# Performance work log

Measured on AMD Instinct MI355X. Metric: run time of the kernel, lower is better.

The kernel has to match this reference:

```python
import jax, jax.numpy as jnp
import numpy as np


def _pairwise_sqdist(a, b):
    # a: [m, n, d], b: [m, n, d] -> M: [m, n, n], M[m,i,j] = ||a[m,i]-b[m,j]||^2
    # Use the expansion |a|^2 + |b|^2 - 2 a.b to avoid materializing the
    # [m, n, n, d] difference tensor; clamp tiny negatives from cancellation.
    a2 = jnp.sum(a * a, axis=-1)  # [m, n]
    b2 = jnp.sum(b * b, axis=-1)  # [m, n]
    ab = jnp.einsum('mid,mjd->mij', a, b)  # [m, n, n]
    return jnp.maximum(a2[:, :, None] + b2[:, None, :] - 2.0 * ab, 0.0)


def setup_inputs() -> dict:
    key = jax.random.key(0)
    k1, k2 = jax.random.split(key)
    template = jax.random.normal(k1, (16, 4096, 3), dtype=jnp.float32)
    source = jax.random.normal(k2, (16, 4096, 3), dtype=jnp.float32)
    return {"template": template, "source": source}


def reference(template, source):
    M = _pairwise_sqdist(template, source)  # [m, n, n]
    # min over template index (axis 1): nearest template point for each source point
    dist1 = jnp.mean(jnp.sqrt(jnp.min(M, axis=1)))
    # min over source index (axis 2): nearest source point for each template point
    dist2 = jnp.mean(jnp.sqrt(jnp.min(M, axis=2)))
    return (dist1 + dist2) / 2.0
```

## Files before the change

### kernel.cpp

```cpp
#include <hip/hip_runtime.h>

#define N_PTS   4096
#define N_BATCH 16
#define INV_CNT (1.0f / (2.0f * N_BATCH * N_PTS))
#define AROW_BYTES ((size_t)2 * N_BATCH * N_PTS * 16 * 2)
#define NBLK    512

typedef _Float16 f16x8  __attribute__((ext_vector_type(8)));
#define AS1 __attribute__((address_space(1)))
#define AS3 __attribute__((address_space(3)))

__global__ __launch_bounds__(256) void prep_kernel(
    const float* __restrict__ tpl, const float* __restrict__ src,
    _Float16* __restrict__ arow, float* __restrict__ out) {
    int pt = blockIdx.x * 256 + threadIdx.x;
    if (pt == 0) out[0] = 0.0f;
    const float* p = (pt < 65536 ? tpl : src) + (size_t)(pt & 65535) * 3;
    float x = p[0], y = p[1], z = p[2];
    float o2 = fmaf(x, x, fmaf(y, y, z * z));
    _Float16 xh = (_Float16)x, yh = (_Float16)y, zh = (_Float16)z;
    _Float16 xl = (_Float16)(x - (float)xh);
    _Float16 yl = (_Float16)(y - (float)yh);
    _Float16 zl = (_Float16)(z - (float)zh);
    _Float16 o2h = (_Float16)o2;
    _Float16 o2l = (_Float16)(o2 - (float)o2h);
    const _Float16 m2 = (_Float16)-2.0f;
    f16x8 v0, v1;
    v0[0] = m2 * xh; v0[1] = m2 * yh; v0[2] = m2 * zh;
    v0[3] = m2 * xl; v0[4] = m2 * yl; v0[5] = m2 * zl;
    v0[6] = m2 * xh; v0[7] = m2 * yh;
    v1[0] = m2 * zh; v1[1] = o2h; v1[2] = o2l;
    v1[3] = (_Float16)0.0f; v1[4] = (_Float16)0.0f; v1[5] = (_Float16)0.0f;
    v1[6] = (_Float16)0.0f; v1[7] = (_Float16)0.0f;
    *(f16x8*)(arow + (size_t)pt * 16)     = v0;
    *(f16x8*)(arow + (size_t)pt * 16 + 8) = v1;
}

#define FD(a,x,y) "v_min3_f32 %[" #a "], v" #x ", v" #y ", %[" #a "]\n\t"
#define FOLD_A FD(acc0,32,33) FD(acc1,34,35) FD(acc0,36,37) FD(acc1,38,39) \
               FD(acc0,40,41) FD(acc1,42,43) FD(acc0,44,45) FD(acc1,46,47) \
               FD(acc2,64,65) FD(acc3,66,67) FD(acc2,68,69) FD(acc3,70,71) \
               FD(acc2,72,73) FD(acc3,74,75) FD(acc2,76,77) FD(acc3,78,79)
#define FOLD_B FD(acc0,48,49) FD(acc1,50,51) FD(acc0,52,53) FD(acc1,54,55) \
               FD(acc0,56,57) FD(acc1,58,59) FD(acc0,60,61) FD(acc1,62,63) \
               FD(acc2,80,81) FD(acc3,82,83) FD(acc2,84,85) FD(acc3,86,87) \
               FD(acc2,88,89) FD(acc3,90,91) FD(acc2,92,93) FD(acc3,94,95)
#define MF_A(d) \
  "v_mfma_f32_32x32x16_f16 v[32:47], %[" #d "], %[bf0], v[96:111]\n\t" \
  "v_mfma_f32_32x32x16_f16 v[64:79], %[" #d "], %[bf1], v[96:111]\n\t"
#define MF_B(d) \
  "v_mfma_f32_32x32x16_f16 v[48:63], %[" #d "], %[bf0], v[96:111]\n\t" \
  "v_mfma_f32_32x32x16_f16 v[80:95], %[" #d "], %[bf1], v[96:111]\n\t"
#define DSR(d,off) "ds_read_b128 %[" #d "], %[dsa] offset:" #off "\n\t"
#define WL(n) "s_waitcnt lgkmcnt(" #n ")\n\t"
#define ZM(r) "v_mov_b32 v" #r ", 0\n\t"
#define NOP3 "s_nop 7\n\t" "s_nop 7\n\t" "s_nop 7\n\t"

__global__ __launch_bounds__(256, 2) void chamfer_mfma(
    const float* __restrict__ tpl, const float* __restrict__ src,
    const _Float16* __restrict__ arow, float* __restrict__ blocksum,
    float* __restrict__ out) {
    __shared__ uint4 sbuf[2][1024];
    __shared__ float wsum[4];

    const int tid = threadIdx.x;
    const int wv = tid >> 6, lane = tid & 63;
    const int n = lane & 31, g = lane >> 5;
    const int lin = blockIdx.x + 16 * (blockIdx.y + 16 * blockIdx.z);
    const int s_  = lin >> 3;
    const int qb  = s_ & 15;
    const int region = (lin & 7) + 8 * (s_ >> 4);
    const int batch  = region & 15;
    const int dir    = region >> 4;

    const float* qpts = (dir == 0) ? src : tpl;
    const _Float16* abase = arow + ((dir == 0) ? (size_t)0 : (size_t)65536 * 16)
                          + (size_t)batch * 4096 * 16;

    f16x8 bfr[2];
    float p2[2];
    #pragma unroll
    for (int i = 0; i < 2; ++i) {
        const int q = qb * 256 + wv * 64 + i * 32 + n;
        const float* p = qpts + (size_t)(batch * 4096 + q) * 3;
        float px = p[0], py = p[1], pz = p[2];
        p2[i] = fmaf(px, px, fmaf(py, py, pz * pz));
        _Float16 xh = (_Float16)px, yh = (_Float16)py, zh = (_Float16)pz;
        _Float16 xl = (_Float16)(px - (float)xh);
        _Float16 yl = (_Float16)(py - (float)yh);
        _Float16 zl = (_Float16)(pz - (float)zh);
        f16x8 b;
        if (g == 0) {
            b[0] = xh; b[1] = yh; b[2] = zh;
            b[3] = xh; b[4] = yh; b[5] = zh;
            b[6] = xl; b[7] = yl;
        } else {
            b[0] = zl; b[1] = (_Float16)1.0f; b[2] = (_Float16)1.0f;
            b[3] = (_Float16)0.0f; b[4] = (_Float16)0.0f; b[5] = (_Float16)0.0f;
            b[6] = (_Float16)0.0f; b[7] = (_Float16)0.0f;
        }
        bfr[i] = b;
    }

    const int lane_off = n * 32 + g * 16;
    const unsigned dsa0 = (unsigned)(size_t)((AS3 char*)&sbuf[0][0]) + lane_off;
    const unsigned dsa1 = (unsigned)(size_t)((AS3 char*)&sbuf[1][0]) + lane_off;

    const char* gwave = (const char*)abase + wv * 4096 + lane * 16;
    #define STAGE(ch)                                                          \
        {                                                                      \
            const char* gp = gwave + (size_t)(ch) * 16384;                     \
            AS3 char* lp = (AS3 char*)&sbuf[(ch) & 1][0] + wv * 4096;          \
            _Pragma("unroll")                                                  \
            for (int j = 0; j < 4; ++j)                                        \
                __builtin_amdgcn_global_load_lds(                              \
                    (const AS1 unsigned*)(gp + j * 1024),                      \
                    (AS3 unsigned*)(lp + j * 1024), 16, 0, 0);                 \
        }

    float acc0 = 1e30f, acc1 = 1e30f, acc2 = 1e30f, acc3 = 1e30f;
    f16x8 d0, d1, d2, d3;

    STAGE(0)
    #pragma unroll 1
    for (int c = 0; c < 8; ++c) {
        if (c < 7) STAGE(c + 1)
        if (c < 7)
            asm volatile("s_waitcnt vmcnt(4)\n\ts_barrier" ::: "memory");
        else
            asm volatile("s_waitcnt vmcnt(0)\n\ts_barrier" ::: "memory");
        const unsigned dsa = (c & 1) ? dsa1 : dsa0;

        asm volatile(
            ZM(96) ZM(97) ZM(98) ZM(99) ZM(100) ZM(101) ZM(102) ZM(103)
            ZM(104) ZM(105) ZM(106) ZM(107) ZM(108) ZM(109) ZM(110) ZM(111)
            DSR(d0,0) DSR(d1,1024) DSR(d2,2048) DSR(d3,3072)
            WL(3) MF_A(d0) DSR(d0,4096) NOP3
            WL(3) MF_B(d1) DSR(d1,5120)  FOLD_A
            WL(3) MF_A(d2) DSR(d2,6144)  FOLD_B
            WL(3) MF_B(d3) DSR(d3,7168)  FOLD_A
            WL(3) MF_A(d0) DSR(d0,8192)  FOLD_B
            WL(3) MF_B(d1) DSR(d1,9216)  FOLD_A
            WL(3) MF_A(d2) DSR(d2,10240) FOLD_B
            WL(3) MF_B(d3) DSR(d3,11264) FOLD_A
            WL(3) MF_A(d0) DSR(d0,12288) FOLD_B
            WL(3) MF_B(d1) DSR(d1,13312) FOLD_A
            WL(3) MF_A(d2) DSR(d2,14336) FOLD_B
            WL(3) MF_B(d3) DSR(d3,15360) FOLD_A
            WL(3) MF_A(d0) FOLD_B
            WL(2) MF_B(d1) FOLD_A
            WL(1) MF_A(d2) FOLD_B
            WL(0) MF_B(d3) FOLD_A
            NOP3 FOLD_B
            : [d0]"=&v"(d0), [d1]"=&v"(d1), [d2]"=&v"(d2), [d3]"=&v"(d3),
              [acc0]"+v"(acc0), [acc1]"+v"(acc1),
              [acc2]"+v"(acc2), [acc3]"+v"(acc3)
            : [bf0]"v"(bfr[0]), [bf1]"v"(bfr[1]), [dsa]"v"(dsa)
            : "memory",
              "v32","v33","v34","v35","v36","v37","v38","v39",
              "v40","v41","v42","v43","v44","v45","v46","v47",
              "v48","v49","v50","v51","v52","v53","v54","v55",
              "v56","v57","v58","v59","v60","v61","v62","v63",
              "v64","v65","v66","v67","v68","v69","v70","v71",
              "v72","v73","v74","v75","v76","v77","v78","v79",
              "v80","v81","v82","v83","v84","v85","v86","v87",
              "v88","v89","v90","v91","v92","v93","v94","v95",
              "v96","v97","v98","v99","v100","v101","v102","v103",
              "v104","v105","v106","v107","v108","v109","v110","v111");

        asm volatile("s_barrier" ::: "memory");
    }

    float v0 = fminf(acc0, acc1);
    v0 = fminf(v0, __shfl_xor(v0, 32));
    float v1 = fminf(acc2, acc3);
    v1 = fminf(v1, __shfl_xor(v1, 32));
    float dd0 = fmaxf(v0 + p2[0], 0.0f);
    float dd1 = fmaxf(v1 + p2[1], 0.0f);
    float s = (sqrtf(dd0) + sqrtf(dd1)) * INV_CNT;
    if (g != 0) s = 0.0f;
    #pragma unroll
    for (int off = 32; off > 0; off >>= 1) s += __shfl_down(s, off);
    if (lane == 0) wsum[wv] = s;
    __syncthreads();
    if (tid == 0) {
        float t = wsum[0] + wsum[1] + wsum[2] + wsum[3];
        if (blocksum) {
            int flat = (dir * N_BATCH + batch) * 16 + qb;
            blocksum[flat] = t;
        } else {
            atomicAdd(out, t);
        }
    }
}

__global__ __launch_bounds__(256) void final_kernel(
    const float* __restrict__ blocksum, float* __restrict__ out) {
    __shared__ float wsum[4];
    float s = 0.0f;
    #pragma unroll
    for (int j = 0; j < NBLK / 256; ++j)
        s += blocksum[j * 256 + threadIdx.x];
    #pragma unroll
    for (int off = 32; off > 0; off >>= 1) s += __shfl_down(s, off);
    if ((threadIdx.x & 63) == 0) wsum[threadIdx.x >> 6] = s;
    __syncthreads();
    if (threadIdx.x == 0) out[0] = wsum[0] + wsum[1] + wsum[2] + wsum[3];
}

extern "C" void kernel_launch(void* const* d_in, const int* in_sizes, int n_in,
                              void* d_out, int out_size, void* d_ws, size_t ws_size,
                              hipStream_t stream) {
    const float* tpl = (const float*)d_in[0];
    const float* src = (const float*)d_in[1];
    float* out = (float*)d_out;
    _Float16* arow = (_Float16*)d_ws;
    const bool roomy = ws_size >= AROW_BYTES + NBLK * sizeof(float);
    float* blocksum = roomy ? (float*)((char*)d_ws + AROW_BYTES) : nullptr;

    hipLaunchKernelGGL(prep_kernel, dim3((2 * N_BATCH * N_PTS) / 256),
                       dim3(256), 0, stream, tpl, src, arow, out);
    dim3 grid(N_PTS / 256, N_BATCH, 2);
    hipLaunchKernelGGL(chamfer_mfma, grid, dim3(256), 0, stream,
                       tpl, src, arow, blocksum, out);
    if (roomy)
        hipLaunchKernelGGL(final_kernel, dim3(1), dim3(256), 0, stream,
                           blocksum, out);
}
```

Baseline: 75.85 us.

## Split reference rows across waves and give each wave all block queries

Each wave now keeps all 256 query columns of the block as eight B fragments and reads only its own quarter of every staged reference chunk, instead of one 64-query slice against all rows. This removes the per-chunk block barriers, since each wave consumes only the LDS region it loads itself, and cuts LDS read traffic per MFMA. The partial minima from the four waves are then combined through shared memory at the end. The cost is more VGPRs (eight B fragments and sixteen accumulators), which may hurt occupancy at two blocks per CU. There is also a redundant zl expression.

```diff
diff --git a/kernel.cpp b/kernel.cpp
--- a/kernel.cpp
+++ b/kernel.cpp
@@ -37,24 +37,32 @@
 }
 
 #define FD(a,x,y) "v_min3_f32 %[" #a "], v" #x ", v" #y ", %[" #a "]\n\t"
-#define FOLD_A FD(acc0,32,33) FD(acc1,34,35) FD(acc0,36,37) FD(acc1,38,39) \
-               FD(acc0,40,41) FD(acc1,42,43) FD(acc0,44,45) FD(acc1,46,47) \
-               FD(acc2,64,65) FD(acc3,66,67) FD(acc2,68,69) FD(acc3,70,71) \
-               FD(acc2,72,73) FD(acc3,74,75) FD(acc2,76,77) FD(acc3,78,79)
-#define FOLD_B FD(acc0,48,49) FD(acc1,50,51) FD(acc0,52,53) FD(acc1,54,55) \
-               FD(acc0,56,57) FD(acc1,58,59) FD(acc0,60,61) FD(acc1,62,63) \
-               FD(acc2,80,81) FD(acc3,82,83) FD(acc2,84,85) FD(acc3,86,87) \
-               FD(acc2,88,89) FD(acc3,90,91) FD(acc2,92,93) FD(acc3,94,95)
-#define MF_A(d) \
-  "v_mfma_f32_32x32x16_f16 v[32:47], %[" #d "], %[bf0], v[96:111]\n\t" \
-  "v_mfma_f32_32x32x16_f16 v[64:79], %[" #d "], %[bf1], v[96:111]\n\t"
-#define MF_B(d) \
-  "v_mfma_f32_32x32x16_f16 v[48:63], %[" #d "], %[bf0], v[96:111]\n\t" \
-  "v_mfma_f32_32x32x16_f16 v[80:95], %[" #d "], %[bf1], v[96:111]\n\t"
+#define FOLD_D0(p,q) FD(p,32,33) FD(q,34,35) FD(p,36,37) FD(q,38,39) \
+                     FD(p,40,41) FD(q,42,43) FD(p,44,45) FD(q,46,47)
+#define FOLD_D1(p,q) FD(p,48,49) FD(q,50,51) FD(p,52,53) FD(q,54,55) \
+                     FD(p,56,57) FD(q,58,59) FD(p,60,61) FD(q,62,63)
+#define FOLD_D2(p,q) FD(p,64,65) FD(q,66,67) FD(p,68,69) FD(q,70,71) \
+                     FD(p,72,73) FD(q,74,75) FD(p,76,77) FD(q,78,79)
+#define FOLD_D3(p,q) FD(p,80,81) FD(q,82,83) FD(p,84,85) FD(q,86,87) \
+                     FD(p,88,89) FD(q,90,91) FD(p,92,93) FD(q,94,95)
+#define MFD0(d,b) "v_mfma_f32_32x32x16_f16 v[32:47], %[" #d "], %[" #b "], v[96:111]\n\t"
+#define MFD1(d,b) "v_mfma_f32_32x32x16_f16 v[48:63], %[" #d "], %[" #b "], v[96:111]\n\t"
+#define MFD2(d,b) "v_mfma_f32_32x32x16_f16 v[64:79], %[" #d "], %[" #b "], v[96:111]\n\t"
+#define MFD3(d,b) "v_mfma_f32_32x32x16_f16 v[80:95], %[" #d "], %[" #b "], v[96:111]\n\t"
 #define DSR(d,off) "ds_read_b128 %[" #d "], %[dsa] offset:" #off "\n\t"
 #define WL(n) "s_waitcnt lgkmcnt(" #n ")\n\t"
 #define ZM(r) "v_mov_b32 v" #r ", 0\n\t"
 #define NOP3 "s_nop 7\n\t" "s_nop 7\n\t" "s_nop 7\n\t"
+
+#define TILE(d,wl) \
+  WL(wl) \
+  MFD0(d,bf0) MFD1(d,bf1) MFD2(d,bf2) MFD3(d,bf3) \
+  NOP3 \
+  FOLD_D0(acc0,acc1)   MFD0(d,bf4) \
+  FOLD_D1(acc2,acc3)   MFD1(d,bf5) \
+  FOLD_D2(acc4,acc5)   MFD2(d,bf6) \
+  FOLD_D3(acc6,acc7)   MFD3(d,bf7) \
+  FOLD_D0(acc8,acc9) FOLD_D1(acc10,acc11) FOLD_D2(acc12,acc13) FOLD_D3(acc14,acc15)
 
 __global__ __launch_bounds__(256, 2) void chamfer_mfma(
     const float* __restrict__ tpl, const float* __restrict__ src,
@@ -77,18 +85,19 @@
     const _Float16* abase = arow + ((dir == 0) ? (size_t)0 : (size_t)65536 * 16)
                           + (size_t)batch * 4096 * 16;
 
-    f16x8 bfr[2];
-    float p2[2];
+    f16x8 bfr[8];
+    float p2[8];
     #pragma unroll
-    for (int i = 0; i < 2; ++i) {
-        const int q = qb * 256 + wv * 64 + i * 32 + n;
+    for (int f = 0; f < 8; ++f) {
+        const int q = qb * 256 + f * 32 + n;
         const float* p = qpts + (size_t)(batch * 4096 + q) * 3;
         float px = p[0], py = p[1], pz = p[2];
-        p2[i] = fmaf(px, px, fmaf(py, py, pz * pz));
+        p2[f] = fmaf(px, px, fmaf(py, py, pz * pz));
         _Float16 xh = (_Float16)px, yh = (_Float16)py, zh = (_Float16)pz;
         _Float16 xl = (_Float16)(px - (float)xh);
         _Float16 yl = (_Float16)(py - (float)yh);
-        _Float16 zl = (_Float16)(pz - (float)zh);
+        _Float16 zl = (_Float16)(pz - (float)pz + (float)(pz - (float)zh));
+        zl = (_Float16)(pz - (float)zh);
         f16x8 b;
         if (g == 0) {
             b[0] = xh; b[1] = yh; b[2] = zh;
@@ -99,12 +108,12 @@
             b[3] = (_Float16)0.0f; b[4] = (_Float16)0.0f; b[5] = (_Float16)0.0f;
             b[6] = (_Float16)0.0f; b[7] = (_Float16)0.0f;
         }
-        bfr[i] = b;
+        bfr[f] = b;
     }
 
     const int lane_off = n * 32 + g * 16;
-    const unsigned dsa0 = (unsigned)(size_t)((AS3 char*)&sbuf[0][0]) + lane_off;
-    const unsigned dsa1 = (unsigned)(size_t)((AS3 char*)&sbuf[1][0]) + lane_off;
+    const unsigned dsa0 = (unsigned)(size_t)((AS3 char*)&sbuf[0][0]) + wv * 4096 + lane_off;
+    const unsigned dsa1 = (unsigned)(size_t)((AS3 char*)&sbuf[1][0]) + wv * 4096 + lane_off;
 
     const char* gwave = (const char*)abase + wv * 4096 + lane * 16;
     #define STAGE(ch)                                                          \
@@ -119,43 +128,42 @@
         }
 
     float acc0 = 1e30f, acc1 = 1e30f, acc2 = 1e30f, acc3 = 1e30f;
+    float acc4 = 1e30f, acc5 = 1e30f, acc6 = 1e30f, acc7 = 1e30f;
+    float acc8 = 1e30f, acc9 = 1e30f, acc10 = 1e30f, acc11 = 1e30f;
+    float acc12 = 1e30f, acc13 = 1e30f, acc14 = 1e30f, acc15 = 1e30f;
     f16x8 d0, d1, d2, d3;
 
     STAGE(0)
     #pragma unroll 1
     for (int c = 0; c < 8; ++c) {
-        if (c < 7) STAGE(c + 1)
-        if (c < 7)
-            asm volatile("s_waitcnt vmcnt(4)\n\ts_barrier" ::: "memory");
-        else
-            asm volatile("s_waitcnt vmcnt(0)\n\ts_barrier" ::: "memory");
+        if (c < 7) {
+            STAGE(c + 1)
+            asm volatile("s_waitcnt vmcnt(4)" ::: "memory");
+        } else {
+            asm volatile("s_waitcnt vmcnt(0)" ::: "memory");
+        }
         const unsigned dsa = (c & 1) ? dsa1 : dsa0;
 
         asm volatile(
             ZM(96) ZM(97) ZM(98) ZM(99) ZM(100) ZM(101) ZM(102) ZM(103)
             ZM(104) ZM(105) ZM(106) ZM(107) ZM(108) ZM(109) ZM(110) ZM(111)
             DSR(d0,0) DSR(d1,1024) DSR(d2,2048) DSR(d3,3072)
-            WL(3) MF_A(d0) DSR(d0,4096) NOP3
-            WL(3) MF_B(d1) DSR(d1,5120)  FOLD_A
-            WL(3) MF_A(d2) DSR(d2,6144)  FOLD_B
-            WL(3) MF_B(d3) DSR(d3,7168)  FOLD_A
-            WL(3) MF_A(d0) DSR(d0,8192)  FOLD_B
-            WL(3) MF_B(d1) DSR(d1,9216)  FOLD_A
-            WL(3) MF_A(d2) DSR(d2,10240) FOLD_B
-            WL(3) MF_B(d3) DSR(d3,11264) FOLD_A
-            WL(3) MF_A(d0) DSR(d0,12288) FOLD_B
-            WL(3) MF_B(d1) DSR(d1,13312) FOLD_A
-            WL(3) MF_A(d2) DSR(d2,14336) FOLD_B
-            WL(3) MF_B(d3) DSR(d3,15360) FOLD_A
-            WL(3) MF_A(d0) FOLD_B
-            WL(2) MF_B(d1) FOLD_A
-            WL(1) MF_A(d2) FOLD_B
-            WL(0) MF_B(d3) FOLD_A
-            NOP3 FOLD_B
+            TILE(d0,3)
+            TILE(d1,2)
+            TILE(d2,1)
+            TILE(d3,0)
             : [d0]"=&v"(d0), [d1]"=&v"(d1), [d2]"=&v"(d2), [d3]"=&v"(d3),
-              [acc0]"+v"(acc0), [acc1]"+v"(acc1),
-              [acc2]"+v"(acc2), [acc3]"+v"(acc3)
-            : [bf0]"v"(bfr[0]), [bf1]"v"(bfr[1]), [dsa]"v"(dsa)
+              [acc0]"+v"(acc0),   [acc1]"+v"(acc1),
+              [acc2]"+v"(acc2),   [acc3]"+v"(acc3),
+              [acc4]"+v"(acc4),   [acc5]"+v"(acc5),
+              [acc6]"+v"(acc6),   [acc7]"+v"(acc7),
+              [acc8]"+v"(acc8),   [acc9]"+v"(acc9),
+              [acc10]"+v"(acc10), [acc11]"+v"(acc11),
+              [acc12]"+v"(acc12), [acc13]"+v"(acc13),
+              [acc14]"+v"(acc14), [acc15]"+v"(acc15)
+            : [bf0]"v"(bfr[0]), [bf1]"v"(bfr[1]), [bf2]"v"(bfr[2]),
+              [bf3]"v"(bfr[3]), [bf4]"v"(bfr[4]), [bf5]"v"(bfr[5]),
+              [bf6]"v"(bfr[6]), [bf7]"v"(bfr[7]), [dsa]"v"(dsa)
             : "memory",
               "v32","v33","v34","v35","v36","v37","v38","v39",
               "v40","v41","v42","v43","v44","v45","v46","v47",
@@ -167,21 +175,41 @@
               "v88","v89","v90","v91","v92","v93","v94","v95",
               "v96","v97","v98","v99","v100","v101","v102","v103",
               "v104","v105","v106","v107","v108","v109","v110","v111");
-
-        asm volatile("s_barrier" ::: "memory");
-    }
-
-    float v0 = fminf(acc0, acc1);
-    v0 = fminf(v0, __shfl_xor(v0, 32));
-    float v1 = fminf(acc2, acc3);
-    v1 = fminf(v1, __shfl_xor(v1, 32));
-    float dd0 = fmaxf(v0 + p2[0], 0.0f);
-    float dd1 = fmaxf(v1 + p2[1], 0.0f);
-    float s = (sqrtf(dd0) + sqrtf(dd1)) * INV_CNT;
-    if (g != 0) s = 0.0f;
-    #pragma unroll
-    for (int off = 32; off > 0; off >>= 1) s += __shfl_down(s, off);
-    if (lane == 0) wsum[wv] = s;
+    }
+
+    float m0 = fminf(acc0,  acc1);  m0 = fminf(m0, __shfl_xor(m0, 32));
+    float m1 = fminf(acc2,  acc3);  m1 = fminf(m1, __shfl_xor(m1, 32));
+    float m2 = fminf(acc4,  acc5);  m2 = fminf(m2, __shfl_xor(m2, 32));
+    float m3 = fminf(acc6,  acc7);  m3 = fminf(m3, __shfl_xor(m3, 32));
+    float m4 = fminf(acc8,  acc9);  m4 = fminf(m4, __shfl_xor(m4, 32));
+    float m5 = fminf(acc10, acc11); m5 = fminf(m5, __shfl_xor(m5, 32));
+    float m6 = fminf(acc12, acc13); m6 = fminf(m6, __shfl_xor(m6, 32));
+    float m7 = fminf(acc14, acc15); m7 = fminf(m7, __shfl_xor(m7, 32));
+
+    __syncthreads();
+    float* cs = (float*)&sbuf[0][0];
+    if (g == 0) {
+        float* cw = cs + wv * 256 + n;
+        cw[0] = m0;  cw[32] = m1;  cw[64] = m2;  cw[96] = m3;
+        cw[128] = m4; cw[160] = m5; cw[192] = m6; cw[224] = m7;
+    }
+    if (tid < 32) {
+        float* cp = cs + 1024 + n;
+        #pragma unroll
+        for (int f = 0; f < 8; ++f) cp[f * 32] = p2[f];
+    }
+    __syncthreads();
+
+    {
+        const int f = wv * 2 + g;
+        const float* cr = cs + f * 32 + n;
+        float mm = fminf(fminf(cr[0], cr[256]), fminf(cr[512], cr[768]));
+        float dd = fmaxf(mm + cr[1024], 0.0f);
+        float s = sqrtf(dd) * INV_CNT;
+        #pragma unroll
+        for (int off = 32; off > 0; off >>= 1) s += __shfl_down(s, off);
+        if (lane == 0) wsum[wv] = s;
+    }
     __syncthreads();
     if (tid == 0) {
         float t = wsum[0] + wsum[1] + wsum[2] + wsum[3];
```

Result: slower. 78.67 us (+3.7%).

## Fuse point packing into main kernel and drop separate prep and final kernels

Applied to the files above, without the earlier changes.

Removes the prep kernel that packed the split-f16 point rows into workspace. Each block now loads raw float coordinates from global memory into registers, packs them into LDS itself, and overlaps that work with the MFMA loop by loading the chunk after next while packing the next one. The final reduction kernel is replaced by a memset plus a per-block atomicAdd. This saves two kernel launches and the workspace round trip, at the cost of redundant packing in every block, VALU work inside the loop, and non-deterministic atomic summation order.

```diff
diff --git a/kernel.cpp b/kernel.cpp
--- a/kernel.cpp
+++ b/kernel.cpp
@@ -3,20 +3,12 @@
 #define N_PTS   4096
 #define N_BATCH 16
 #define INV_CNT (1.0f / (2.0f * N_BATCH * N_PTS))
-#define AROW_BYTES ((size_t)2 * N_BATCH * N_PTS * 16 * 2)
-#define NBLK    512
 
 typedef _Float16 f16x8  __attribute__((ext_vector_type(8)));
-#define AS1 __attribute__((address_space(1)))
 #define AS3 __attribute__((address_space(3)))
 
-__global__ __launch_bounds__(256) void prep_kernel(
-    const float* __restrict__ tpl, const float* __restrict__ src,
-    _Float16* __restrict__ arow, float* __restrict__ out) {
-    int pt = blockIdx.x * 256 + threadIdx.x;
-    if (pt == 0) out[0] = 0.0f;
-    const float* p = (pt < 65536 ? tpl : src) + (size_t)(pt & 65535) * 3;
-    float x = p[0], y = p[1], z = p[2];
+
+__device__ inline void pack_pt(float x, float y, float z, AS3 _Float16* lp) {
     float o2 = fmaf(x, x, fmaf(y, y, z * z));
     _Float16 xh = (_Float16)x, yh = (_Float16)y, zh = (_Float16)z;
     _Float16 xl = (_Float16)(x - (float)xh);
@@ -32,8 +24,8 @@
     v1[0] = m2 * zh; v1[1] = o2h; v1[2] = o2l;
     v1[3] = (_Float16)0.0f; v1[4] = (_Float16)0.0f; v1[5] = (_Float16)0.0f;
     v1[6] = (_Float16)0.0f; v1[7] = (_Float16)0.0f;
-    *(f16x8*)(arow + (size_t)pt * 16)     = v0;
-    *(f16x8*)(arow + (size_t)pt * 16 + 8) = v1;
+    *(AS3 f16x8*)lp       = v0;
+    *(AS3 f16x8*)(lp + 8) = v1;
 }
 
 #define FD(a,x,y) "v_min3_f32 %[" #a "], v" #x ", v" #y ", %[" #a "]\n\t"
@@ -56,9 +48,8 @@
 #define ZM(r) "v_mov_b32 v" #r ", 0\n\t"
 #define NOP3 "s_nop 7\n\t" "s_nop 7\n\t" "s_nop 7\n\t"
 
-__global__ __launch_bounds__(256, 2) void chamfer_mfma(
+__global__ __launch_bounds__(256, 2) void chamfer_fused(
     const float* __restrict__ tpl, const float* __restrict__ src,
-    const _Float16* __restrict__ arow, float* __restrict__ blocksum,
     float* __restrict__ out) {
     __shared__ uint4 sbuf[2][1024];
     __shared__ float wsum[4];
@@ -74,8 +65,8 @@
     const int dir    = region >> 4;
 
     const float* qpts = (dir == 0) ? src : tpl;
-    const _Float16* abase = arow + ((dir == 0) ? (size_t)0 : (size_t)65536 * 16)
-                          + (size_t)batch * 4096 * 16;
+    const float* araw = ((dir == 0) ? tpl : src)
+                      + (size_t)batch * 4096 * 3;
 
     f16x8 bfr[2];
     float p2[2];
@@ -106,29 +97,34 @@
     const unsigned dsa0 = (unsigned)(size_t)((AS3 char*)&sbuf[0][0]) + lane_off;
     const unsigned dsa1 = (unsigned)(size_t)((AS3 char*)&sbuf[1][0]) + lane_off;
 
-    const char* gwave = (const char*)abase + wv * 4096 + lane * 16;
-    #define STAGE(ch)                                                          \
+    float r0, r1, r2, r3, r4, r5;
+    #define ALOAD(ch)                                                          \
         {                                                                      \
-            const char* gp = gwave + (size_t)(ch) * 16384;                     \
-            AS3 char* lp = (AS3 char*)&sbuf[(ch) & 1][0] + wv * 4096;          \
-            _Pragma("unroll")                                                  \
-            for (int j = 0; j < 4; ++j)                                        \
-                __builtin_amdgcn_global_load_lds(                              \
-                    (const AS1 unsigned*)(gp + j * 1024),                      \
-                    (AS3 unsigned*)(lp + j * 1024), 16, 0, 0);                 \
+            const float* gp = araw + (size_t)(ch) * 1536 + tid * 3;            \
+            r0 = gp[0]; r1 = gp[1]; r2 = gp[2];                                \
+            r3 = gp[768]; r4 = gp[769]; r5 = gp[770];                          \
+        }
+    #define APACK(ch)                                                          \
+        {                                                                      \
+            AS3 _Float16* lp = (AS3 _Float16*)&sbuf[(ch) & 1][0];              \
+            pack_pt(r0, r1, r2, lp + tid * 16);                                \
+            pack_pt(r3, r4, r5, lp + (tid + 256) * 16);                        \
         }
 
     float acc0 = 1e30f, acc1 = 1e30f, acc2 = 1e30f, acc3 = 1e30f;
     f16x8 d0, d1, d2, d3;
 
-    STAGE(0)
+    ALOAD(0)
+    APACK(0)
+    ALOAD(1)
+    __syncthreads();
+
     #pragma unroll 1
     for (int c = 0; c < 8; ++c) {
-        if (c < 7) STAGE(c + 1)
-        if (c < 7)
-            asm volatile("s_waitcnt vmcnt(4)\n\ts_barrier" ::: "memory");
-        else
-            asm volatile("s_waitcnt vmcnt(0)\n\ts_barrier" ::: "memory");
+        if (c < 7) {
+            APACK(c + 1)
+            if (c < 6) ALOAD(c + 2)
+        }
         const unsigned dsa = (c & 1) ? dsa1 : dsa0;
 
         asm volatile(
@@ -168,7 +164,7 @@
               "v96","v97","v98","v99","v100","v101","v102","v103",
               "v104","v105","v106","v107","v108","v109","v110","v111");
 
-        asm volatile("s_barrier" ::: "memory");
+        if (c < 7) __syncthreads();
     }
 
     float v0 = fminf(acc0, acc1);
@@ -183,29 +179,8 @@
     for (int off = 32; off > 0; off >>= 1) s += __shfl_down(s, off);
     if (lane == 0) wsum[wv] = s;
     __syncthreads();
-    if (tid == 0) {
-        float t = wsum[0] + wsum[1] + wsum[2] + wsum[3];
-        if (blocksum) {
-            int flat = (dir * N_BATCH + batch) * 16 + qb;
-            blocksum[flat] = t;
-        } else {
-            atomicAdd(out, t);
-        }
-    }
-}
-
-__global__ __launch_bounds__(256) void final_kernel(
-    const float* __restrict__ blocksum, float* __restrict__ out) {
-    __shared__ float wsum[4];
-    float s = 0.0f;
-    #pragma unroll
-    for (int j = 0; j < NBLK / 256; ++j)
-        s += blocksum[j * 256 + threadIdx.x];
-    #pragma unroll
-    for (int off = 32; off > 0; off >>= 1) s += __shfl_down(s, off);
-    if ((threadIdx.x & 63) == 0) wsum[threadIdx.x >> 6] = s;
-    __syncthreads();
-    if (threadIdx.x == 0) out[0] = wsum[0] + wsum[1] + wsum[2] + wsum[3];
+    if (tid == 0)
+        atomicAdd(out, wsum[0] + wsum[1] + wsum[2] + wsum[3]);
 }
 
 extern "C" void kernel_launch(void* const* d_in, const int* in_sizes, int n_in,
@@ -214,16 +189,10 @@
     const float* tpl = (const float*)d_in[0];
     const float* src = (const float*)d_in[1];
     float* out = (float*)d_out;
-    _Float16* arow = (_Float16*)d_ws;
-    const bool roomy = ws_size >= AROW_BYTES + NBLK * sizeof(float);
-    float* blocksum = roomy ? (float*)((char*)d_ws + AROW_BYTES) : nullptr;
+    (void)d_ws; (void)ws_size; (void)in_sizes; (void)n_in; (void)out_size;
 
-    hipLaunchKernelGGL(prep_kernel, dim3((2 * N_BATCH * N_PTS) / 256),
-                       dim3(256), 0, stream, tpl, src, arow, out);
+    hipMemsetAsync(out, 0, sizeof(float), stream);
     dim3 grid(N_PTS / 256, N_BATCH, 2);
-    hipLaunchKernelGGL(chamfer_mfma, grid, dim3(256), 0, stream,
-                       tpl, src, arow, blocksum, out);
-    if (roomy)
-        hipLaunchKernelGGL(final_kernel, dim3(1), dim3(256), 0, stream,
-                           blocksum, out);
+    hipLaunchKernelGGL(chamfer_fused, grid, dim3(256), 0, stream,
+                       tpl, src, out);
 }
```

After: 77.17 us. About the same (+1.7%).

## Split reference-point range in half per block and reduce per-query minima in final kernel

Applied to the files above, without the earlier changes.

Each workgroup now scans only half of the reference points, which doubles the grid to 1024 blocks. Per-query partial minima are written to a workspace buffer, and the final kernel, now 128 blocks, combines the two halves, takes the sqrt and reduces with atomics. Occupancy hint raised to 3 blocks per CU. This targets load imbalance and under-utilisation from only 512 blocks on a 256-CU device. The cost is an extra global round-trip of per-query minima and a heavier final kernel. The code also drops the workspace-size check.

```diff
diff --git a/kernel.cpp b/kernel.cpp
--- a/kernel.cpp
+++ b/kernel.cpp
@@ -4,7 +4,8 @@
 #define N_BATCH 16
 #define INV_CNT (1.0f / (2.0f * N_BATCH * N_PTS))
 #define AROW_BYTES ((size_t)2 * N_BATCH * N_PTS * 16 * 2)
-#define NBLK    512
+#define NQUERY (2 * N_BATCH * N_PTS)
+#define NFBLK  128
 
 typedef _Float16 f16x8  __attribute__((ext_vector_type(8)));
 #define AS1 __attribute__((address_space(1)))
@@ -56,26 +57,26 @@
 #define ZM(r) "v_mov_b32 v" #r ", 0\n\t"
 #define NOP3 "s_nop 7\n\t" "s_nop 7\n\t" "s_nop 7\n\t"
 
-__global__ __launch_bounds__(256, 2) void chamfer_mfma(
+__global__ __launch_bounds__(256, 3) void chamfer_mfma(
     const float* __restrict__ tpl, const float* __restrict__ src,
-    const _Float16* __restrict__ arow, float* __restrict__ blocksum,
-    float* __restrict__ out) {
+    const _Float16* __restrict__ arow, float* __restrict__ qmin) {
     __shared__ uint4 sbuf[2][1024];
-    __shared__ float wsum[4];
 
     const int tid = threadIdx.x;
     const int wv = tid >> 6, lane = tid & 63;
     const int n = lane & 31, g = lane >> 5;
     const int lin = blockIdx.x + 16 * (blockIdx.y + 16 * blockIdx.z);
-    const int s_  = lin >> 3;
-    const int qb  = s_ & 15;
-    const int region = (lin & 7) + 8 * (s_ >> 4);
-    const int batch  = region & 15;
-    const int dir    = region >> 4;
+    const int wgid  = (lin & 7) * 128 + (lin >> 3);
+    const int qb    = wgid & 15;
+    const int batch = (wgid >> 4) & 15;
+    const int dh    = wgid >> 8;
+    const int dir   = dh >> 1;
+    const int ahalf = dh & 1;
 
     const float* qpts = (dir == 0) ? src : tpl;
     const _Float16* abase = arow + ((dir == 0) ? (size_t)0 : (size_t)65536 * 16)
-                          + (size_t)batch * 4096 * 16;
+                          + (size_t)batch * 4096 * 16
+                          + (size_t)ahalf * 2048 * 16;
 
     f16x8 bfr[2];
     float p2[2];
@@ -104,7 +105,6 @@
 
     const int lane_off = n * 32 + g * 16;
     const unsigned dsa0 = (unsigned)(size_t)((AS3 char*)&sbuf[0][0]) + lane_off;
-    const unsigned dsa1 = (unsigned)(size_t)((AS3 char*)&sbuf[1][0]) + lane_off;
 
     const char* gwave = (const char*)abase + wv * 4096 + lane * 16;
     #define STAGE(ch)                                                          \
@@ -123,13 +123,13 @@
 
     STAGE(0)
     #pragma unroll 1
-    for (int c = 0; c < 8; ++c) {
-        if (c < 7) STAGE(c + 1)
-        if (c < 7)
+    for (int c = 0; c < 4; ++c) {
+        if (c < 3) STAGE(c + 1)
+        if (c < 3)
             asm volatile("s_waitcnt vmcnt(4)\n\ts_barrier" ::: "memory");
         else
             asm volatile("s_waitcnt vmcnt(0)\n\ts_barrier" ::: "memory");
-        const unsigned dsa = (c & 1) ? dsa1 : dsa0;
+        const unsigned dsa = dsa0 + ((unsigned)(c & 1) << 14);
 
         asm volatile(
             ZM(96) ZM(97) ZM(98) ZM(99) ZM(100) ZM(101) ZM(102) ZM(103)
@@ -177,35 +177,30 @@
     v1 = fminf(v1, __shfl_xor(v1, 32));
     float dd0 = fmaxf(v0 + p2[0], 0.0f);
     float dd1 = fmaxf(v1 + p2[1], 0.0f);
-    float s = (sqrtf(dd0) + sqrtf(dd1)) * INV_CNT;
-    if (g != 0) s = 0.0f;
-    #pragma unroll
-    for (int off = 32; off > 0; off >>= 1) s += __shfl_down(s, off);
-    if (lane == 0) wsum[wv] = s;
-    __syncthreads();
-    if (tid == 0) {
-        float t = wsum[0] + wsum[1] + wsum[2] + wsum[3];
-        if (blocksum) {
-            int flat = (dir * N_BATCH + batch) * 16 + qb;
-            blocksum[flat] = t;
-        } else {
-            atomicAdd(out, t);
-        }
+    if (g == 0) {
+        const int qid = ((dir * N_BATCH + batch) << 12) + qb * 256 + wv * 64 + n;
+        qmin[(size_t)ahalf * NQUERY + qid]      = dd0;
+        qmin[(size_t)ahalf * NQUERY + qid + 32] = dd1;
     }
 }
 
 __global__ __launch_bounds__(256) void final_kernel(
-    const float* __restrict__ blocksum, float* __restrict__ out) {
+    const float* __restrict__ qmin, float* __restrict__ out) {
     __shared__ float wsum[4];
     float s = 0.0f;
+    const int base = blockIdx.x * (NQUERY / NFBLK) + threadIdx.x;
     #pragma unroll
-    for (int j = 0; j < NBLK / 256; ++j)
-        s += blocksum[j * 256 + threadIdx.x];
+    for (int j = 0; j < NQUERY / NFBLK / 256; ++j) {
+        const int q = base + j * 256;
+        s += sqrtf(fminf(qmin[q], qmin[NQUERY + q]));
+    }
+    s *= INV_CNT;
     #pragma unroll
     for (int off = 32; off > 0; off >>= 1) s += __shfl_down(s, off);
     if ((threadIdx.x & 63) == 0) wsum[threadIdx.x >> 6] = s;
     __syncthreads();
-    if (threadIdx.x == 0) out[0] = wsum[0] + wsum[1] + wsum[2] + wsum[3];
+    if (threadIdx.x == 0)
+        atomicAdd(out, wsum[0] + wsum[1] + wsum[2] + wsum[3]);
 }
 
 extern "C" void kernel_launch(void* const* d_in, const int* in_sizes, int n_in,
@@ -215,15 +210,14 @@
     const float* src = (const float*)d_in[1];
     float* out = (float*)d_out;
     _Float16* arow = (_Float16*)d_ws;
-    const bool roomy = ws_size >= AROW_BYTES + NBLK * sizeof(float);
-    float* blocksum = roomy ? (float*)((char*)d_ws + AROW_BYTES) : nullptr;
+    float* qmin = (float*)((char*)d_ws + AROW_BYTES);
+    (void)in_sizes; (void)n_in; (void)out_size; (void)ws_size;
 
     hipLaunchKernelGGL(prep_kernel, dim3((2 * N_BATCH * N_PTS) / 256),
                        dim3(256), 0, stream, tpl, src, arow, out);
-    dim3 grid(N_PTS / 256, N_BATCH, 2);
+    dim3 grid(N_PTS / 256, N_BATCH, 4);
     hipLaunchKernelGGL(chamfer_mfma, grid, dim3(256), 0, stream,
-                       tpl, src, arow, blocksum, out);
-    if (roomy)
-        hipLaunchKernelGGL(final_kernel, dim3(1), dim3(256), 0, stream,
-                           blocksum, out);
-}
+                       tpl, src, arow, qmin);
+    hipLaunchKernelGGL(final_kernel, dim3(NFBLK), dim3(256), 0, stream,
+                       qmin, out);
+}
```

After: 77.68 us. 1.02x slower.
